# Kernel optimization log

Measured on AMD Instinct MI355X. Metric: run time of the kernel, lower is better.

## Reference

```python
import jax, jax.numpy as jnp
import numpy as np

BITS = 4
MAXQ = (1 << BITS) - 1  # 15
GROUPSIZE = 128
IN_F = 8192
OUT_F = 8192
PACK = 32 // BITS  # 8 values per int32


def setup_inputs() -> dict:
    key = jax.random.key(0)
    k_x, k_w, k_z, k_s, k_b = jax.random.split(key, 5)
    groups = IN_F // GROUPSIZE
    x = jax.random.normal(k_x, (4, 32, IN_F), dtype=jnp.float32)
    # bit-packed int32 weight / zeros (random bit patterns are valid quantized data)
    qweight = jax.random.randint(k_w, (IN_F // PACK, OUT_F), 0, 2**31 - 1, dtype=jnp.int32)
    qzeros = jax.random.randint(k_z, (groups, OUT_F // PACK), 0, 2**31 - 1, dtype=jnp.int32)
    scales = (jax.random.uniform(k_s, (groups, OUT_F), dtype=jnp.float32) * 0.01 + 1e-3)
    g_idx = (jnp.arange(IN_F, dtype=jnp.int32) // GROUPSIZE).astype(jnp.int32)
    bias = jax.random.normal(k_b, (OUT_F,), dtype=jnp.float32) * 0.01
    return {"x": x, "qweight": qweight, "qzeros": qzeros, "scales": scales,
            "g_idx": g_idx, "bias": bias}


def _dequant(qweight, qzeros, scales, g_idx):
    shifts = jnp.arange(0, 32, BITS, dtype=jnp.int32)  # [PACK]
    # unpack weights along the input dim: [in/PACK, PACK, out] -> [in, out]
    w = (qweight[:, None, :] >> shifts[None, :, None]) & MAXQ
    w = w.reshape(-1, qweight.shape[1])
    # unpack zeros along the output dim: [groups, out/PACK, PACK] -> [groups, out]
    # GPTQ stores (zero - 1), so add 1 back
    z = ((qzeros[:, :, None] >> shifts[None, None, :]) & MAXQ) + 1
    z = z.reshape(qzeros.shape[0], -1)
    # per-group dequant: W[i, o] = scales[g_idx[i], o] * (w[i, o] - z[g_idx[i], o])
    W = scales[g_idx] * (w.astype(scales.dtype) - z[g_idx].astype(scales.dtype))
    return W  # [in, out]


def reference(x, qweight, qzeros, scales, g_idx, bias):
    W = _dequant(qweight, qzeros, scales, g_idx)
    out = jnp.einsum('bsi,io->bso', x, W) + bias
    return out
```

## Files before the change

### kernel.cpp

```cpp
#include <hip/hip_runtime.h>
#include <hip/hip_bf16.h>
#include <stdint.h>


#define IN_F 8192
#define OUT_F 8192
#define MROWS 128

typedef short short8_t __attribute__((ext_vector_type(8)));
typedef float float4_t __attribute__((ext_vector_type(4)));
typedef float float16_t __attribute__((ext_vector_type(16)));

template<int NSL>
__global__ void reduce_out(const unsigned short* __restrict__ part,
                           const float* __restrict__ bias,
                           float* __restrict__ out) {
  const int i = (blockIdx.x * 256 + threadIdx.x) * 8;
  const int o = i & (OUT_F - 1);
  float4_t s0 = *(const float4_t*)(bias + o);
  float4_t s1 = *(const float4_t*)(bias + o + 4);
#pragma unroll
  for (int sl = 0; sl < NSL; ++sl) {
    union { uint4 u; unsigned short us[8]; } p;
    p.u = *(const uint4*)(part + (size_t)sl * MROWS * OUT_F + i);
    s0.x += __uint_as_float((unsigned)p.us[0] << 16);
    s0.y += __uint_as_float((unsigned)p.us[1] << 16);
    s0.z += __uint_as_float((unsigned)p.us[2] << 16);
    s0.w += __uint_as_float((unsigned)p.us[3] << 16);
    s1.x += __uint_as_float((unsigned)p.us[4] << 16);
    s1.y += __uint_as_float((unsigned)p.us[5] << 16);
    s1.z += __uint_as_float((unsigned)p.us[6] << 16);
    s1.w += __uint_as_float((unsigned)p.us[7] << 16);
  }
  *(float4_t*)(out + i)     = s0;
  *(float4_t*)(out + i + 4) = s1;
}

__global__ __launch_bounds__(1024, 8) void gptq_gemm_ks16(
    const float* __restrict__ x,
    const int* __restrict__ qweight,
    const int* __restrict__ qzeros,
    const float* __restrict__ scales,
    unsigned short* __restrict__ part)
{
  __shared__ unsigned short As[64 * 512];

  const int tid  = threadIdx.x;
  const int lane = tid & 63;
  const int l31  = lane & 31;
  const int half = lane >> 5;
  const int wv   = tid >> 6;

  const int bid = blockIdx.x;
  const int kb  = bid >> 5;
  const int mb  = (bid >> 4) & 1;
  const int nb  = bid & 15;

  const int kc0 = kb * 512;
  const int m0  = mb * 64;
  const int g0  = kc0 >> 7;
  const int kp_base = (kc0 >> 3) + half;

  const int col = nb * 512 + wv * 32 + l31;

  int   qw[3][8];
  float sc[3];
  int   zq[3];

  auto prefetch = [&](int i, int buf) {
    const int kp = kp_base + i * 16;
#pragma unroll
    for (int ks = 0; ks < 8; ++ks)
      qw[buf][ks] = qweight[(size_t)(kp + ks * 2) * OUT_F + col];
    const int gg_abs = g0 + i;
    sc[buf] = scales[gg_abs * OUT_F + col];
    zq[buf] = qzeros[gg_abs * (OUT_F / 8) + (col >> 3)];
  };

  prefetch(0, 0);
  prefetch(1, 1);

  for (int rq = 0; rq < 4; ++rq) {
    const int rl = wv * 4 + rq;
    const float* grow = x + (size_t)(m0 + rl) * IN_F + kc0;
    const int p = lane;
    const int c = (p & ~15) | ((p ^ (rl & 15)) & 15);
    float4_t a = *(const float4_t*)(grow + c * 8);
    float4_t b = *(const float4_t*)(grow + c * 8 + 4);
    union { short8_t v; __hip_bfloat162 h[4]; } u;
    u.h[0] = __float22bfloat162_rn(make_float2(a.x, a.y));
    u.h[1] = __float22bfloat162_rn(make_float2(a.z, a.w));
    u.h[2] = __float22bfloat162_rn(make_float2(b.x, b.y));
    u.h[3] = __float22bfloat162_rn(make_float2(b.z, b.w));
    *(short8_t*)(As + ((size_t)rl * 64 + p) * 8) = u.v;
  }
  __syncthreads();

  float16_t acc[2];
#pragma unroll
  for (int mt = 0; mt < 2; ++mt)
#pragma unroll
    for (int r = 0; r < 16; ++r) acc[mt][r] = 0.f;

#pragma unroll
  for (int g = 0; g < 4; ++g) {
    const int cur = g % 3;

    if (g + 2 < 4) prefetch(g + 2, (g + 2) % 3);

    const int z = ((zq[cur] >> (4 * (col & 7))) & 15) + 1;
    const float zb = -sc[cur] * (float)z;
    const float s = sc[cur];

#pragma unroll
    for (int ks = 0; ks < 8; ++ks) {
      const int c = g * 16 + ks * 2 + half;
      const int p = (c & ~15) | ((c ^ (l31 & 15)) & 15);

      short8_t af[2];
#pragma unroll
      for (int mt = 0; mt < 2; ++mt)
        af[mt] = *(const short8_t*)(As + ((size_t)(mt * 32 + l31) * 64 + p) * 8);

      union { short8_t v; unsigned u[4]; } bw;
      const unsigned q  = (unsigned)qw[cur][ks];
      const unsigned qe = q & 0x0F0F0F0Fu;
      const unsigned qo = (q >> 4) & 0x0F0F0F0Fu;
#pragma unroll
      for (int jj = 0; jj < 4; ++jj) {
        const float f0 = fmaf(s, (float)((qe >> (8 * jj)) & 0xffu), zb);
        const float f1 = fmaf(s, (float)((qo >> (8 * jj)) & 0xffu), zb);
        bw.u[jj] = __builtin_amdgcn_perm(__float_as_uint(f1), __float_as_uint(f0),
                                         0x07060302u);
      }

#pragma unroll
      for (int mt = 0; mt < 2; ++mt)
        acc[mt] = __builtin_amdgcn_mfma_f32_32x32x16_bf16(af[mt], bw.v, acc[mt], 0, 0, 0);
    }
  }

  unsigned short* base = part + (size_t)kb * (MROWS * OUT_F);
#pragma unroll
  for (int mt = 0; mt < 2; ++mt)
#pragma unroll
    for (int r = 0; r < 16; ++r) {
      const int row = (r & 3) + 8 * (r >> 2) + 4 * half;
      __hip_bfloat16 h = __float2bfloat16(acc[mt][r]);
      base[(size_t)(m0 + mt * 32 + row) * OUT_F + col] = *(unsigned short*)&h;
    }
}

__global__ __launch_bounds__(1024, 4) void gptq_gemm_ks8(
    const float* __restrict__ x,
    const int* __restrict__ qweight,
    const int* __restrict__ qzeros,
    const float* __restrict__ scales,
    unsigned short* __restrict__ part)
{
  __shared__ unsigned short As[64 * 1024];

  const int tid  = threadIdx.x;
  const int lane = tid & 63;
  const int l31  = lane & 31;
  const int half = lane >> 5;
  const int wv   = tid >> 6;

  const int bid = blockIdx.x;
  const int kb  = bid >> 5;
  const int mb  = (bid >> 4) & 1;
  const int nb  = bid & 15;

  const int kc0 = kb * 1024;
  const int m0  = mb * 64;
  const int g0  = kc0 >> 7;
  const int kp_base = (kc0 >> 3) + half;

  const int col = nb * 512 + wv * 32 + l31;

  int   qw[3][8];
  float sc[3];
  int   zq[3];

  auto prefetch = [&](int i, int buf) {
    const int kp = kp_base + i * 16;
#pragma unroll
    for (int ks = 0; ks < 8; ++ks)
      qw[buf][ks] = qweight[(size_t)(kp + ks * 2) * OUT_F + col];
    const int gg_abs = g0 + i;
    sc[buf] = scales[gg_abs * OUT_F + col];
    zq[buf] = qzeros[gg_abs * (OUT_F / 8) + (col >> 3)];
  };

  prefetch(0, 0);
  prefetch(1, 1);

  for (int rq = 0; rq < 4; ++rq) {
    const int rl = wv * 4 + rq;
    const float* grow = x + (size_t)(m0 + rl) * IN_F + kc0;
#pragma unroll
    for (int hf = 0; hf < 2; ++hf) {
      const int p = hf * 64 + lane;
      const int c = (p & 0x70) | ((p ^ (rl & 15)) & 15);
      float4_t a = *(const float4_t*)(grow + c * 8);
      float4_t b = *(const float4_t*)(grow + c * 8 + 4);
      union { short8_t v; __hip_bfloat162 h[4]; } u;
      u.h[0] = __float22bfloat162_rn(make_float2(a.x, a.y));
      u.h[1] = __float22bfloat162_rn(make_float2(a.z, a.w));
      u.h[2] = __float22bfloat162_rn(make_float2(b.x, b.y));
      u.h[3] = __float22bfloat162_rn(make_float2(b.z, b.w));
      *(short8_t*)(As + ((size_t)rl * 128 + p) * 8) = u.v;
    }
  }
  __syncthreads();

  float16_t acc[2];
#pragma unroll
  for (int mt = 0; mt < 2; ++mt)
#pragma unroll
    for (int r = 0; r < 16; ++r) acc[mt][r] = 0.f;

#pragma unroll
  for (int g = 0; g < 8; ++g) {
    const int cur = g % 3;

    if (g + 2 < 8) prefetch(g + 2, (g + 2) % 3);

    const int z = ((zq[cur] >> (4 * (col & 7))) & 15) + 1;
    const float zb = -sc[cur] * (float)z;
    const float s = sc[cur];

#pragma unroll
    for (int ks = 0; ks < 8; ++ks) {
      const int c = g * 16 + ks * 2 + half;
      const int p = (c & 0x70) | ((c ^ (l31 & 15)) & 15);

      short8_t af[2];
#pragma unroll
      for (int mt = 0; mt < 2; ++mt)
        af[mt] = *(const short8_t*)(As + ((size_t)(mt * 32 + l31) * 128 + p) * 8);

      union { short8_t v; unsigned u[4]; } bw;
      const unsigned q  = (unsigned)qw[cur][ks];
      const unsigned qe = q & 0x0F0F0F0Fu;
      const unsigned qo = (q >> 4) & 0x0F0F0F0Fu;
#pragma unroll
      for (int jj = 0; jj < 4; ++jj) {
        const float f0 = fmaf(s, (float)((qe >> (8 * jj)) & 0xffu), zb);
        const float f1 = fmaf(s, (float)((qo >> (8 * jj)) & 0xffu), zb);
        bw.u[jj] = __builtin_amdgcn_perm(__float_as_uint(f1), __float_as_uint(f0),
                                         0x07060302u);
      }

#pragma unroll
      for (int mt = 0; mt < 2; ++mt)
        acc[mt] = __builtin_amdgcn_mfma_f32_32x32x16_bf16(af[mt], bw.v, acc[mt], 0, 0, 0);
    }
  }

  unsigned short* base = part + (size_t)kb * (MROWS * OUT_F);
#pragma unroll
  for (int mt = 0; mt < 2; ++mt)
#pragma unroll
    for (int r = 0; r < 16; ++r) {
      const int row = (r & 3) + 8 * (r >> 2) + 4 * half;
      __hip_bfloat16 h = __float2bfloat16(acc[mt][r]);
      base[(size_t)(m0 + mt * 32 + row) * OUT_F + col] = *(unsigned short*)&h;
    }
}

extern "C" void kernel_launch(void* const* d_in, const int* in_sizes, int n_in,
                              void* d_out, int out_size, void* d_ws, size_t ws_size,
                              hipStream_t stream) {
  const float* x        = (const float*)d_in[0];
  const int*   qweight  = (const int*)d_in[1];
  const int*   qzeros   = (const int*)d_in[2];
  const float* scales   = (const float*)d_in[3];
  const float* bias     = (const float*)d_in[5];
  float* out = (float*)d_out;

  unsigned short* part = (unsigned short*)d_ws;

  const size_t need16 = (size_t)16 * MROWS * OUT_F * sizeof(unsigned short);
  if (ws_size >= need16) {
    gptq_gemm_ks16<<<dim3(512), 1024, 0, stream>>>(x, qweight, qzeros, scales, part);
    reduce_out<16><<<dim3((MROWS * OUT_F) / (256 * 8)), 256, 0, stream>>>(part, bias, out);
  } else {
    gptq_gemm_ks8<<<dim3(256), 1024, 0, stream>>>(x, qweight, qzeros, scales, part);
    reduce_out<8><<<dim3((MROWS * OUT_F) / (256 * 8)), 256, 0, stream>>>(part, bias, out);
  }
}
```

Measured before the change: 122.4 us.

## Split K into 256-wide chunks with 512-thread blocks and 32 partial slices

The main GEMM kernel now processes 256-wide K chunks over 256 output columns with 512-thread blocks, launching 2048 blocks instead of 512. All quantized weights for the chunk are loaded up front, and the triple-buffered rolling prefetch is removed. The reduction kernel now sums 32 bf16 partial slices instead of 16. This raises parallelism and occupancy with smaller LDS per block, at the cost of twice the partial-sum traffic and reduction work, plus a larger workspace requirement.

Measured after the change: 128.0 us. 1.05x slower.

```diff
diff --git a/kernel.cpp b/kernel.cpp
--- a/kernel.cpp
+++ b/kernel.cpp
@@ -36,14 +36,14 @@
   *(float4_t*)(out + i + 4) = s1;
 }
 
-__global__ __launch_bounds__(1024, 8) void gptq_gemm_ks16(
+__global__ __launch_bounds__(512, 6) void gptq_gemm_k256(
     const float* __restrict__ x,
     const int* __restrict__ qweight,
     const int* __restrict__ qzeros,
     const float* __restrict__ scales,
     unsigned short* __restrict__ part)
 {
-  __shared__ unsigned short As[64 * 512];
+  __shared__ unsigned short As[64 * 256];
 
   const int tid  = threadIdx.x;
   const int lane = tid & 63;
@@ -52,38 +52,34 @@
   const int wv   = tid >> 6;
 
   const int bid = blockIdx.x;
-  const int kb  = bid >> 5;
-  const int mb  = (bid >> 4) & 1;
-  const int nb  = bid & 15;
-
-  const int kc0 = kb * 512;
+  const int kb  = bid >> 6;
+  const int mb  = (bid >> 5) & 1;
+  const int nb  = bid & 31;
+
+  const int kc0 = kb * 256;
   const int m0  = mb * 64;
   const int g0  = kc0 >> 7;
   const int kp_base = (kc0 >> 3) + half;
 
-  const int col = nb * 512 + wv * 32 + l31;
-
-  int   qw[3][8];
-  float sc[3];
-  int   zq[3];
-
-  auto prefetch = [&](int i, int buf) {
-    const int kp = kp_base + i * 16;
+  const int col = nb * 256 + wv * 32 + l31;
+
+  int   qw[2][8];
+  float sc[2];
+  int   zq[2];
+#pragma unroll
+  for (int g = 0; g < 2; ++g) {
+    const int kp = kp_base + g * 16;
 #pragma unroll
     for (int ks = 0; ks < 8; ++ks)
-      qw[buf][ks] = qweight[(size_t)(kp + ks * 2) * OUT_F + col];
-    const int gg_abs = g0 + i;
-    sc[buf] = scales[gg_abs * OUT_F + col];
-    zq[buf] = qzeros[gg_abs * (OUT_F / 8) + (col >> 3)];
-  };
-
-  prefetch(0, 0);
-  prefetch(1, 1);
+      qw[g][ks] = qweight[(size_t)(kp + ks * 2) * OUT_F + col];
+    sc[g] = scales[(g0 + g) * OUT_F + col];
+    zq[g] = qzeros[(g0 + g) * (OUT_F / 8) + (col >> 3)];
+  }
 
   for (int rq = 0; rq < 4; ++rq) {
-    const int rl = wv * 4 + rq;
+    const int rl = wv * 8 + rq * 2 + half;
     const float* grow = x + (size_t)(m0 + rl) * IN_F + kc0;
-    const int p = lane;
+    const int p = l31;
     const int c = (p & ~15) | ((p ^ (rl & 15)) & 15);
     float4_t a = *(const float4_t*)(grow + c * 8);
     float4_t b = *(const float4_t*)(grow + c * 8 + 4);
@@ -92,7 +88,7 @@
     u.h[1] = __float22bfloat162_rn(make_float2(a.z, a.w));
     u.h[2] = __float22bfloat162_rn(make_float2(b.x, b.y));
     u.h[3] = __float22bfloat162_rn(make_float2(b.z, b.w));
-    *(short8_t*)(As + ((size_t)rl * 64 + p) * 8) = u.v;
+    *(short8_t*)(As + ((size_t)rl * 32 + p) * 8) = u.v;
   }
   __syncthreads();
 
@@ -103,14 +99,10 @@
     for (int r = 0; r < 16; ++r) acc[mt][r] = 0.f;
 
 #pragma unroll
-  for (int g = 0; g < 4; ++g) {
-    const int cur = g % 3;
-
-    if (g + 2 < 4) prefetch(g + 2, (g + 2) % 3);
-
-    const int z = ((zq[cur] >> (4 * (col & 7))) & 15) + 1;
-    const float zb = -sc[cur] * (float)z;
-    const float s = sc[cur];
+  for (int g = 0; g < 2; ++g) {
+    const int z = ((zq[g] >> (4 * (col & 7))) & 15) + 1;
+    const float zb = -sc[g] * (float)z;
+    const float s = sc[g];
 
 #pragma unroll
     for (int ks = 0; ks < 8; ++ks) {
@@ -120,10 +112,10 @@
       short8_t af[2];
 #pragma unroll
       for (int mt = 0; mt < 2; ++mt)
-        af[mt] = *(const short8_t*)(As + ((size_t)(mt * 32 + l31) * 64 + p) * 8);
+        af[mt] = *(const short8_t*)(As + ((size_t)(mt * 32 + l31) * 32 + p) * 8);
 
       union { short8_t v; unsigned u[4]; } bw;
-      const unsigned q  = (unsigned)qw[cur][ks];
+      const unsigned q  = (unsigned)qw[g][ks];
       const unsigned qe = q & 0x0F0F0F0Fu;
       const unsigned qo = (q >> 4) & 0x0F0F0F0Fu;
 #pragma unroll
@@ -281,10 +273,10 @@
 
   unsigned short* part = (unsigned short*)d_ws;
 
-  const size_t need16 = (size_t)16 * MROWS * OUT_F * sizeof(unsigned short);
-  if (ws_size >= need16) {
-    gptq_gemm_ks16<<<dim3(512), 1024, 0, stream>>>(x, qweight, qzeros, scales, part);
-    reduce_out<16><<<dim3((MROWS * OUT_F) / (256 * 8)), 256, 0, stream>>>(part, bias, out);
+  const size_t need32 = (size_t)32 * MROWS * OUT_F * sizeof(unsigned short);
+  if (ws_size >= need32) {
+    gptq_gemm_k256<<<dim3(2048), 512, 0, stream>>>(x, qweight, qzeros, scales, part);
+    reduce_out<32><<<dim3((MROWS * OUT_F) / (256 * 8)), 256, 0, stream>>>(part, bias, out);
   } else {
     gptq_gemm_ks8<<<dim3(256), 1024, 0, stream>>>(x, qweight, qzeros, scales, part);
     reduce_out<8><<<dim3((MROWS * OUT_F) / (256 * 8)), 256, 0, stream>>>(part, bias, out);
```

## Halve block size and loop each wave over two column tiles

Applied to the files above, without the earlier changes.

The split-K GEMM block drops from 1024 to 512 threads, and each wave now processes two 32-column tiles in sequence (8 iterations instead of 4), writing partial sums after each tile. Each block stages 64 rows of x into shared memory with 8 rows per wave, and that LDS A tile is reused across both column tiles. Prefetching goes from triple to double buffering to cut register use. The intent is to lower the cost of staging A per unit of work and to let more blocks fit per CU, at the cost of less latency hiding per wave.

After: 155.0 us. +26.6%, slower.

```diff
diff --git a/kernel.cpp b/kernel.cpp
--- a/kernel.cpp
+++ b/kernel.cpp
@@ -36,7 +36,7 @@
   *(float4_t*)(out + i + 4) = s1;
 }
 
-__global__ __launch_bounds__(1024, 8) void gptq_gemm_ks16(
+__global__ __launch_bounds__(512, 4) void gptq_gemm_pers(
     const float* __restrict__ x,
     const int* __restrict__ qweight,
     const int* __restrict__ qzeros,
@@ -54,34 +54,34 @@
   const int bid = blockIdx.x;
   const int kb  = bid >> 5;
   const int mb  = (bid >> 4) & 1;
-  const int nb  = bid & 15;
+  const int nbs = bid & 15;
 
   const int kc0 = kb * 512;
   const int m0  = mb * 64;
   const int g0  = kc0 >> 7;
   const int kp_base = (kc0 >> 3) + half;
 
-  const int col = nb * 512 + wv * 32 + l31;
-
-  int   qw[3][8];
-  float sc[3];
-  int   zq[3];
-
-  auto prefetch = [&](int i, int buf) {
-    const int kp = kp_base + i * 16;
+  const int colbase = nbs * 512 + wv * 32 + l31;
+
+  int   qw[2][8];
+  float sc[2];
+  int   zq[2];
+
+  auto prefetch = [&](int t, int buf) {
+    const int g    = t & 3;
+    const int colt = colbase + (t >> 2) * 256;
+    sc[buf] = scales[(g0 + g) * OUT_F + colt];
+    zq[buf] = qzeros[(g0 + g) * (OUT_F / 8) + (colt >> 3)];
+    const int kp = kp_base + g * 16;
 #pragma unroll
     for (int ks = 0; ks < 8; ++ks)
-      qw[buf][ks] = qweight[(size_t)(kp + ks * 2) * OUT_F + col];
-    const int gg_abs = g0 + i;
-    sc[buf] = scales[gg_abs * OUT_F + col];
-    zq[buf] = qzeros[gg_abs * (OUT_F / 8) + (col >> 3)];
+      qw[buf][ks] = qweight[(size_t)(kp + ks * 2) * OUT_F + colt];
   };
 
   prefetch(0, 0);
-  prefetch(1, 1);
-
-  for (int rq = 0; rq < 4; ++rq) {
-    const int rl = wv * 4 + rq;
+
+  for (int rq = 0; rq < 8; ++rq) {
+    const int rl = wv * 8 + rq;
     const float* grow = x + (size_t)(m0 + rl) * IN_F + kc0;
     const int p = lane;
     const int c = (p & ~15) | ((p ^ (rl & 15)) & 15);
@@ -102,13 +102,16 @@
 #pragma unroll
     for (int r = 0; r < 16; ++r) acc[mt][r] = 0.f;
 
-#pragma unroll
-  for (int g = 0; g < 4; ++g) {
-    const int cur = g % 3;
-
-    if (g + 2 < 4) prefetch(g + 2, (g + 2) % 3);
-
-    const int z = ((zq[cur] >> (4 * (col & 7))) & 15) + 1;
+  unsigned short* const pbase = part + (size_t)kb * (MROWS * OUT_F);
+
+#pragma unroll
+  for (int t = 0; t < 8; ++t) {
+    const int cur = t & 1;
+    const int g   = t & 3;
+
+    if (t + 1 < 8) prefetch(t + 1, cur ^ 1);
+
+    const int z = ((zq[cur] >> (4 * (colbase & 7))) & 15) + 1;
     const float zb = -sc[cur] * (float)z;
     const float s = sc[cur];
 
@@ -138,17 +141,20 @@
       for (int mt = 0; mt < 2; ++mt)
         acc[mt] = __builtin_amdgcn_mfma_f32_32x32x16_bf16(af[mt], bw.v, acc[mt], 0, 0, 0);
     }
-  }
-
-  unsigned short* base = part + (size_t)kb * (MROWS * OUT_F);
-#pragma unroll
-  for (int mt = 0; mt < 2; ++mt)
-#pragma unroll
-    for (int r = 0; r < 16; ++r) {
-      const int row = (r & 3) + 8 * (r >> 2) + 4 * half;
-      __hip_bfloat16 h = __float2bfloat16(acc[mt][r]);
-      base[(size_t)(m0 + mt * 32 + row) * OUT_F + col] = *(unsigned short*)&h;
-    }
+
+    if ((t & 3) == 3) {
+      const int colt = colbase + (t >> 2) * 256;
+#pragma unroll
+      for (int mt = 0; mt < 2; ++mt)
+#pragma unroll
+        for (int r = 0; r < 16; ++r) {
+          const int row = (r & 3) + 8 * (r >> 2) + 4 * half;
+          __hip_bfloat16 h = __float2bfloat16(acc[mt][r]);
+          pbase[(size_t)(m0 + mt * 32 + row) * OUT_F + colt] = *(unsigned short*)&h;
+          acc[mt][r] = 0.f;
+        }
+    }
+  }
 }
 
 __global__ __launch_bounds__(1024, 4) void gptq_gemm_ks8(
@@ -283,7 +289,7 @@
 
   const size_t need16 = (size_t)16 * MROWS * OUT_F * sizeof(unsigned short);
   if (ws_size >= need16) {
-    gptq_gemm_ks16<<<dim3(512), 1024, 0, stream>>>(x, qweight, qzeros, scales, part);
+    gptq_gemm_pers<<<dim3(512), 512, 0, stream>>>(x, qweight, qzeros, scales, part);
     reduce_out<16><<<dim3((MROWS * OUT_F) / (256 * 8)), 256, 0, stream>>>(part, bias, out);
   } else {
     gptq_gemm_ks8<<<dim3(256), 1024, 0, stream>>>(x, qweight, qzeros, scales, part);
```
